# Kernel tuning notes

Hardware: AMD Instinct MI355X
Metric: run time of the kernel (lower is better)

The kernel has to match this reference:

```python
import jax, jax.numpy as jnp
import numpy as np
from jax import lax

CAP_N = 3
ROUTE_NUM = 3


def squash(s, axis=-1):
    # v = (|s|^2 / (1+|s|^2)) * s / |s|
    n2 = jnp.sum(s * s, axis=axis, keepdims=True)
    return (n2 / (1.0 + n2)) * s * lax.rsqrt(n2 + 1e-8)


def cap_layer2(x, W, bias, b0, num_out_caps, out_dim, as_final):
    # x: [bs, in_dim, H, W]; W: [out_dim*num_out_caps, in_dim] (1x1 conv)
    bs = x.shape[0]
    pred = jnp.einsum('oc,bchw->bohw', W, x) + bias[None, :, None, None]
    pred = pred.reshape(bs, num_out_caps, out_dim, -1)      # [bs, out_caps, d, in_caps]
    pred = jnp.transpose(pred, (0, 3, 1, 2))                # [bs, in_caps, out_caps, d]
    b = b0                                                   # [bs, out_caps, in_caps]
    v = None
    for _ in range(ROUTE_NUM):
        c = jax.nn.softmax(b, axis=1)                        # softmax over out_caps
        s = jnp.einsum('boi,biod->bod', c, pred)             # [bs, out_caps, d]
        v = squash(s)
        db = lax.stop_gradient(jnp.einsum('bod,biod->boi', v, pred))
        b = b + db
    if not as_final:
        side = int(np.sqrt(num_out_caps))
        v = jnp.transpose(v, (0, 2, 1)).reshape(bs, out_dim, side, side)
    return v


def setup_inputs() -> dict:
    key = jax.random.key(0)
    ks = jax.random.split(key, 8)
    bs = 128
    x = jax.random.normal(ks[0], (bs, 64, 8, 8), dtype=jnp.float32)
    Wb = jax.random.normal(ks[1], (64, 64, 3, 3), dtype=jnp.float32) * 0.05
    bb = jnp.zeros((64,), dtype=jnp.float32)
    W1 = jax.random.normal(ks[2], (4096, 64), dtype=jnp.float32) * 0.05
    b1 = jnp.zeros((4096,), dtype=jnp.float32)
    W2 = jax.random.normal(ks[3], (640, 64), dtype=jnp.float32) * 0.05
    b2 = jnp.zeros((640,), dtype=jnp.float32)
    b_basic = jax.random.uniform(ks[4], (CAP_N, bs, 64, 64), dtype=jnp.float32)
    b_cls = jax.random.uniform(ks[5], (bs, 10, 64), dtype=jnp.float32)
    return {'x': x, 'Wb': Wb, 'bb': bb, 'W1': W1, 'b1': b1, 'W2': W2, 'b2': b2,
            'b_basic': b_basic, 'b_cls': b_cls}


def reference(x, Wb, bb, W1, b1, W2, b2, b_basic, b_cls):
    # buffer: 3x3 conv + ReLU
    h = lax.conv_general_dilated(x, Wb, (1, 1), 'SAME',
                                 dimension_numbers=('NCHW', 'OIHW', 'NCHW'))
    h = jax.nn.relu(h + bb[None, :, None, None])
    # _do_squash over channel dim per spatial location
    h = squash(h, axis=1)
    for i in range(CAP_N):
        h = cap_layer2(h, W1, b1, b_basic[i], 64, 64, False)
    v = cap_layer2(h, W2, b2, b_cls, 10, 64, True)   # [bs, 10, 64]
    return v
```

## Files before the change

### kernel.cpp

```cpp
#include <hip/hip_runtime.h>
#include <math.h>
#include <type_traits>


#define SYS_ST(p, v) __hip_atomic_store((p), (v), __ATOMIC_RELAXED, __HIP_MEMORY_SCOPE_SYSTEM)
#define SYS_LD(p)    __hip_atomic_load((p), __ATOMIC_RELAXED, __HIP_MEMORY_SCOPE_SYSTEM)

typedef float v4f __attribute__((ext_vector_type(4)));

__device__ __forceinline__ void sys_st4(float* p, float4 q) {
    v4f v; v[0] = q.x; v[1] = q.y; v[2] = q.z; v[3] = q.w;
    asm volatile("global_store_dwordx4 %0, %1, off sc0 sc1" :: "v"(p), "v"(v) : "memory");
}

__global__ __launch_bounds__(512) void prep_kernel(
    const float* __restrict__ x, const float* __restrict__ Wb,
    const float* __restrict__ bb,
    const float* __restrict__ W1, const float* __restrict__ b1,
    const float* __restrict__ W2, const float* __restrict__ b2,
    const float* __restrict__ b_basic,
    float* __restrict__ h,
    float* __restrict__ WT1, float* __restrict__ G1,
    float* __restrict__ gb1, float* __restrict__ bb21,
    float* __restrict__ WT2, float* __restrict__ G2,
    float* __restrict__ gb2, float* __restrict__ bb22,
    float* __restrict__ den0, int* __restrict__ flags)
{
    __shared__ float smem[10560];
    const int blk = blockIdx.x;
    const int t = threadIdx.x;

    if (blk < 128) {
        float* xs  = smem;
        float* hs  = smem + 6400;
        float* scl = smem + 10496;
        const int b = blk;
        for (int idx = t; idx < 6400; idx += 512) xs[idx] = 0.f;
        __syncthreads();
        #pragma unroll
        for (int k = 0; k < 2; ++k) {
            int idx4 = t + k * 512;
            float4 v = *(const float4*)&x[(size_t)b * 4096 + idx4 * 4];
            int e0 = idx4 * 4;
            int c  = e0 >> 6;
            int hw = e0 & 63;
            int r = hw >> 3, cc = hw & 7;
            float* xp = &xs[c * 100 + (r + 1) * 10 + (cc + 1)];
            xp[0] = v.x; xp[1] = v.y; xp[2] = v.z; xp[3] = v.w;
        }
        __syncthreads();
        const int oc = t >> 3;
        const int hg = t & 7;
        float acc[8];
        #pragma unroll
        for (int k = 0; k < 8; ++k) acc[k] = 0.f;
        const float* wp = Wb + (size_t)oc * 576;
        for (int ic = 0; ic < 64; ++ic) {
            float w[9];
            #pragma unroll
            for (int j = 0; j < 9; ++j) w[j] = wp[ic * 9 + j];
            const float* xr = &xs[ic * 100];
            #pragma unroll
            for (int k = 0; k < 8; ++k) {
                int hw = hg * 8 + k;
                int r = hw >> 3, cc = hw & 7;
                int p0 = r * 10 + cc;
                float a = acc[k];
                a = fmaf(w[0], xr[p0],      a);
                a = fmaf(w[1], xr[p0 + 1],  a);
                a = fmaf(w[2], xr[p0 + 2],  a);
                a = fmaf(w[3], xr[p0 + 10], a);
                a = fmaf(w[4], xr[p0 + 11], a);
                a = fmaf(w[5], xr[p0 + 12], a);
                a = fmaf(w[6], xr[p0 + 20], a);
                a = fmaf(w[7], xr[p0 + 21], a);
                a = fmaf(w[8], xr[p0 + 22], a);
                acc[k] = a;
            }
        }
        float bias = bb[oc];
        #pragma unroll
        for (int k = 0; k < 8; ++k) {
            float v = acc[k] + bias;
            hs[oc * 64 + hg * 8 + k] = v > 0.f ? v : 0.f;
        }
        __syncthreads();
        if (t < 64) {
            float n2 = 0.f;
            for (int c = 0; c < 64; ++c) { float v = hs[c * 64 + t]; n2 = fmaf(v, v, n2); }
            scl[t] = (n2 / (1.f + n2)) * rsqrtf(n2 + 1e-8f);
        }
        __syncthreads();
        #pragma unroll
        for (int k = 0; k < 2; ++k) {
            int idx4 = t + k * 512;
            int e0 = idx4 * 4;
            int hw0 = e0 & 63;
            float4 o;
            o.x = hs[e0 + 0] * scl[hw0 + 0];
            o.y = hs[e0 + 1] * scl[hw0 + 1];
            o.z = hs[e0 + 2] * scl[hw0 + 2];
            o.w = hs[e0 + 3] * scl[hw0 + 3];
            *(float4*)&h[(size_t)b * 4096 + e0] = o;
        }
    } else if (blk < 202) {
        const bool w1 = blk < 192;
        const int o = w1 ? (blk - 128) : (blk - 192);
        const float* W    = w1 ? W1 : W2;
        const float* bias = w1 ? b1 : b2;
        float* WT  = w1 ? WT1  : WT2;
        float* G   = w1 ? G1   : G2;
        float* gb  = w1 ? gb1  : gb2;
        float* bb2 = w1 ? bb21 : bb22;
        float* WS = smem;
        if (t < 256) {
            #pragma unroll
            for (int p = 0; p < 4; ++p) {
                int idx = t + p * 256;
                int d = idx >> 4, c0 = (idx & 15) * 4;
                *(float4*)&WS[d * 68 + c0] =
                    *(const float4*)&W[((size_t)o * 64 + d) * 64 + c0];
            }
        }
        __syncthreads();
        if (t < 256) {
            {
                const int Q = t & 15, R = t >> 4;
                #pragma unroll
                for (int p = 0; p < 4; ++p) {
                    int c = R + 16 * p;
                    float4 v;
                    v.x = WS[(4 * Q + 0) * 68 + c];
                    v.y = WS[(4 * Q + 1) * 68 + c];
                    v.z = WS[(4 * Q + 2) * 68 + c];
                    v.w = WS[(4 * Q + 3) * 68 + c];
                    *(float4*)&WT[((size_t)o * 64 + c) * 64 + 4 * Q] = v;
                }
            }
            {
                const int c1 = t >> 2, j = t & 3;
                float acc[16];
                #pragma unroll
                for (int g = 0; g < 16; ++g) acc[g] = 0.f;
                for (int d = 0; d < 64; ++d) {
                    float a = WS[d * 68 + c1];
                    #pragma unroll
                    for (int g = 0; g < 16; ++g)
                        acc[g] = fmaf(a, WS[d * 68 + j * 16 + g], acc[g]);
                }
                #pragma unroll
                for (int g = 0; g < 16; ++g)
                    G[(size_t)o * 4096 + c1 * 64 + j * 16 + g] = acc[g];
            }
            if (t < 64) {
                float s = 0.f;
                for (int d = 0; d < 64; ++d) s = fmaf(bias[o * 64 + d], WS[d * 68 + t], s);
                gb[o * 64 + t] = s;
            }
            if (t == 0) {
                float s = 0.f;
                for (int d = 0; d < 64; ++d) { float bv = bias[o * 64 + d]; s = fmaf(bv, bv, s); }
                bb2[o] = s;
            }
        }
    } else if (blk < 250) {
        const int g = (blk - 202) * 512 + t;
        const int L = g >> 13, b = (g >> 6) & 127, i = g & 63;
        const float* bp = b_basic + (((size_t)L * 128 + b) << 12) + i;
        float s = 0.f;
        for (int o = 0; o < 64; ++o) s += expf(bp[o * 64]);
        den0[((size_t)L * 128 + b) * 64 + i] = s;
    } else {
        for (int i = t; i < 4096; i += 512) flags[i] = 0;
    }
}

__global__ __launch_bounds__(1024, 4) void caps_fused(
    const float* __restrict__ h0,
    const float* __restrict__ WT1, const float* __restrict__ G1,
    const float* __restrict__ gb1, const float* __restrict__ bb21,
    const float* __restrict__ b1,
    const float* __restrict__ WT2, const float* __restrict__ G2,
    const float* __restrict__ gb2, const float* __restrict__ bb22,
    const float* __restrict__ b2,
    const float* __restrict__ b_basic, const float* __restrict__ b_cls,
    const float* __restrict__ den0,
    float* __restrict__ xbuf,
    float* __restrict__ vbuf,
    int*   __restrict__ flags,
    float* __restrict__ out)
{
    __shared__ float HC[8704];
    __shared__ float CC[2048];
    __shared__ float PP[10240];

    const int B    = blockIdx.x;
    const int q    = B >> 6;
    const int p    = B & 63;
    const int t    = threadIdx.x;
    const int wv   = t >> 6;
    const int lane = t & 63;
    const int Q    = lane & 15;
    const int GG   = lane >> 4;
    int step = 1, dcnt = 0;

    #pragma unroll
    for (int s = 0; s < 2; ++s) {
        float4 v = *(const float4*)&h0[(size_t)(2 * p + s) * 4096 + t * 4];
        int c = t >> 4, i0 = (t & 15) * 4;
        *(float4*)&HC[s * 4352 + c * 68 + i0] = v;
    }

    auto layer = [&](auto finc, const float* __restrict__ WT,
                     const float* __restrict__ Gm,
                     const float* __restrict__ gbp,
                     const float* __restrict__ bb2p,
                     const float* __restrict__ biasp,
                     const float* __restrict__ bsrc,
                     const float* __restrict__ den0p, bool entry) {
        constexpr bool FIN = decltype(finc)::value;
        const int o   = FIN ? wv : q * 16 + wv;
        const bool act = !FIN || wv < 10;
        const int row0 = (wv * 2) * 64, row1 = (wv * 2 + 1) * 64;

        float bl0 = 0.f, bl1 = 0.f, bb2o = 0.f;
        float4 gbv4 = make_float4(0.f, 0.f, 0.f, 0.f);
        float4 bias4 = gbv4;
        const float* pG  = Gm;
        const float* pWT = WT;
        if (act) {
            pG  = Gm + o * 4096 + GG * 64 + 4 * Q;
            pWT = WT + o * 4096 + GG * 64 + 4 * Q;
            gbv4 = *(const float4*)&gbp[o * 64 + 4 * Q];
            bb2o = bb2p[o];
            bias4 = *(const float4*)&biasp[o * 64 + 4 * Q];
            if (FIN) {
                bl0 = b_cls[(size_t)(2 * p) * 640 + o * 64 + lane];
                bl1 = b_cls[(size_t)(2 * p + 1) * 640 + o * 64 + lane];
            } else {
                bl0 = bsrc[o * 64 + lane];
                bl1 = bsrc[4096 + o * 64 + lane];
            }
        }

        if (entry) {
            if (t < 3) {
                int qq = t + (t >= q);
                while (SYS_LD(&flags[(qq * 64 + p) * 16]) < step) {}
            }
            __syncthreads();
            #pragma unroll
            for (int j = 0; j < 3; ++j) {
                int qq = j + (j >= q);
                const float* vp = vbuf + (size_t)(qq * 64 + p) * 2048;
                #pragma unroll
                for (int rep = 0; rep < 2; ++rep) {
                    int idx = rep * 1024 + t;
                    int d = idx & 63, s = (idx >> 6) & 1, ol = idx >> 7;
                    HC[s * 4352 + d * 68 + qq * 16 + ol] = SYS_LD(&vp[idx]);
                }
            }
            ++step;
            __syncthreads();
        } else {
            __syncthreads();
        }

        for (int it = 0; it < 3; ++it) {
            float cc0 = 0.f, cc1 = 0.f, bp0 = 1.f, bp1 = 1.f;
            if (act) { cc0 = expf(bl0); cc1 = expf(bl1); }
            if (it == 0 && !FIN) {
                if (act) { bp0 = den0p[lane]; bp1 = den0p[64 + lane]; }
            } else {
                PP[wv * 64 + lane] = cc0;
                PP[1024 + wv * 64 + lane] = cc1;
                __syncthreads();
                bp0 = 0.f; bp1 = 0.f;
                #pragma unroll
                for (int w = 0; w < 16; ++w) {
                    bp0 += PP[w * 64 + lane];
                    bp1 += PP[1024 + w * 64 + lane];
                }
                if (!FIN) {
                    float* xb = xbuf + ((size_t)(dcnt & 1) * 256 + B) * 128;
                    if (wv == 0) {
                        SYS_ST(&xb[lane], bp0);
                        SYS_ST(&xb[64 + lane], bp1);
                        asm volatile("s_waitcnt vmcnt(0)" ::: "memory");
                        if (lane == 0) SYS_ST(&flags[B * 16], step);
                        if (lane < 3) {
                            int qq = lane + (lane >= q);
                            while (SYS_LD(&flags[(qq * 64 + p) * 16]) < step) {}
                        }
                    }
                    __syncthreads();
                    #pragma unroll
                    for (int j = 0; j < 3; ++j) {
                        int qq = j + (j >= q);
                        const float* xp = xbuf + ((size_t)(dcnt & 1) * 256 + qq * 64 + p) * 128;
                        bp0 += SYS_LD(&xp[lane]);
                        bp1 += SYS_LD(&xp[64 + lane]);
                    }
                    ++step; ++dcnt;
                }
            }
            float sc0 = 0.f, sc1 = 0.f;
            if (act) {
                float cv0 = cc0 / bp0, cv1 = cc1 / bp1;
                CC[row0 + lane] = cv0;
                CC[row1 + lane] = cv1;
                float a0 = cv0, a1 = cv1;
                #pragma unroll
                for (int m = 1; m < 64; m <<= 1) {
                    a0 += __shfl_xor(a0, m, 64);
                    a1 += __shfl_xor(a1, m, 64);
                }
                sc0 = a0; sc1 = a1;
            }
            __builtin_amdgcn_wave_barrier();

            float y0 = 0.f, y1 = 0.f;
            if (act) {
                #pragma unroll 8
                for (int k = 0; k < 16; ++k) {
                    float4 h40 = *(const float4*)&HC[lane * 68 + 4 * k];
                    float4 c40 = *(const float4*)&CC[row0 + 4 * k];
                    y0 = fmaf(h40.x, c40.x, y0); y0 = fmaf(h40.y, c40.y, y0);
                    y0 = fmaf(h40.z, c40.z, y0); y0 = fmaf(h40.w, c40.w, y0);
                    float4 h41 = *(const float4*)&HC[4352 + lane * 68 + 4 * k];
                    float4 c41 = *(const float4*)&CC[row1 + 4 * k];
                    y1 = fmaf(h41.x, c41.x, y1); y1 = fmaf(h41.y, c41.y, y1);
                    y1 = fmaf(h41.z, c41.z, y1); y1 = fmaf(h41.w, c41.w, y1);
                }
            }
            __builtin_amdgcn_wave_barrier();
            if (act) { CC[row0 + lane] = y0; CC[row1 + lane] = y1; }
            __builtin_amdgcn_wave_barrier();

            if (it < 2) {
                float4 a0 = make_float4(0.f, 0.f, 0.f, 0.f), a1 = a0;
                if (act) {
                    #pragma unroll 8
                    for (int k = 0; k < 16; ++k) {
                        float4 w4 = *(const float4*)&pG[k << 8];
                        float yb0 = CC[row0 + 4 * k + GG];
                        float yb1 = CC[row1 + 4 * k + GG];
                        a0.x = fmaf(w4.x, yb0, a0.x); a0.y = fmaf(w4.y, yb0, a0.y);
                        a0.z = fmaf(w4.z, yb0, a0.z); a0.w = fmaf(w4.w, yb0, a0.w);
                        a1.x = fmaf(w4.x, yb1, a1.x); a1.y = fmaf(w4.y, yb1, a1.y);
                        a1.z = fmaf(w4.z, yb1, a1.z); a1.w = fmaf(w4.w, yb1, a1.w);
                    }
                    #pragma unroll
                    for (int m = 16; m <= 32; m <<= 1) {
                        a0.x += __shfl_xor(a0.x, m, 64); a0.y += __shfl_xor(a0.y, m, 64);
                        a0.z += __shfl_xor(a0.z, m, 64); a0.w += __shfl_xor(a0.w, m, 64);
                        a1.x += __shfl_xor(a1.x, m, 64); a1.y += __shfl_xor(a1.y, m, 64);
                        a1.z += __shfl_xor(a1.z, m, 64); a1.w += __shfl_xor(a1.w, m, 64);
                    }
                }
                float vd0 = 0.f, vd1 = 0.f;
                if (act) {
                    float4 y40 = *(const float4*)&CC[row0 + 4 * Q];
                    float4 y41 = *(const float4*)&CC[row1 + 4 * Q];
                    float n20 = y40.x * a0.x + y40.y * a0.y + y40.z * a0.z + y40.w * a0.w;
                    float n21 = y41.x * a1.x + y41.y * a1.y + y41.z * a1.z + y41.w * a1.w;
                    float yg0 = y40.x * gbv4.x + y40.y * gbv4.y + y40.z * gbv4.z + y40.w * gbv4.w;
                    float yg1 = y41.x * gbv4.x + y41.y * gbv4.y + y41.z * gbv4.z + y41.w * gbv4.w;
                    #pragma unroll
                    for (int m = 1; m <= 8; m <<= 1) {
                        n20 += __shfl_xor(n20, m, 64);
                        n21 += __shfl_xor(n21, m, 64);
                        yg0 += __shfl_xor(yg0, m, 64);
                        yg1 += __shfl_xor(yg1, m, 64);
                    }
                    n20 = n20 + 2.f * sc0 * yg0 + sc0 * sc0 * bb2o;
                    n21 = n21 + 2.f * sc1 * yg1 + sc1 * sc1 * bb2o;
                    float s0 = (n20 / (1.f + n20)) * rsqrtf(n20 + 1e-8f);
                    float s1 = (n21 / (1.f + n21)) * rsqrtf(n21 + 1e-8f);
                    vd0 = s0 * (yg0 + sc0 * bb2o);
                    vd1 = s1 * (yg1 + sc1 * bb2o);
                    if (GG == 0) {
                        float4 u0, u1;
                        u0.x = s0 * (a0.x + sc0 * gbv4.x); u0.y = s0 * (a0.y + sc0 * gbv4.y);
                        u0.z = s0 * (a0.z + sc0 * gbv4.z); u0.w = s0 * (a0.w + sc0 * gbv4.w);
                        u1.x = s1 * (a1.x + sc1 * gbv4.x); u1.y = s1 * (a1.y + sc1 * gbv4.y);
                        u1.z = s1 * (a1.z + sc1 * gbv4.z); u1.w = s1 * (a1.w + sc1 * gbv4.w);
                        *(float4*)&CC[row0 + 4 * Q] = u0;
                        *(float4*)&CC[row1 + 4 * Q] = u1;
                    }
                }
                __builtin_amdgcn_wave_barrier();

                if (act) {
                    float4 d0 = make_float4(0.f, 0.f, 0.f, 0.f), d1 = d0;
                    #pragma unroll 8
                    for (int k = 0; k < 16; ++k) {
                        int c = 4 * k + GG;
                        float4 hc0 = *(const float4*)&HC[c * 68 + 4 * Q];
                        float ub0 = CC[row0 + c];
                        d0.x = fmaf(ub0, hc0.x, d0.x); d0.y = fmaf(ub0, hc0.y, d0.y);
                        d0.z = fmaf(ub0, hc0.z, d0.z); d0.w = fmaf(ub0, hc0.w, d0.w);
                        float4 hc1 = *(const float4*)&HC[4352 + c * 68 + 4 * Q];
                        float ub1 = CC[row1 + c];
                        d1.x = fmaf(ub1, hc1.x, d1.x); d1.y = fmaf(ub1, hc1.y, d1.y);
                        d1.z = fmaf(ub1, hc1.z, d1.z); d1.w = fmaf(ub1, hc1.w, d1.w);
                    }
                    #pragma unroll
                    for (int m = 16; m <= 32; m <<= 1) {
                        d0.x += __shfl_xor(d0.x, m, 64); d0.y += __shfl_xor(d0.y, m, 64);
                        d0.z += __shfl_xor(d0.z, m, 64); d0.w += __shfl_xor(d0.w, m, 64);
                        d1.x += __shfl_xor(d1.x, m, 64); d1.y += __shfl_xor(d1.y, m, 64);
                        d1.z += __shfl_xor(d1.z, m, 64); d1.w += __shfl_xor(d1.w, m, 64);
                    }
                    if (GG == 0) {
                        *(float4*)&CC[row0 + 4 * Q] = d0;
                        *(float4*)&CC[row1 + 4 * Q] = d1;
                    }
                }
                __builtin_amdgcn_wave_barrier();
                if (act) {
                    bl0 += CC[row0 + lane] + vd0;
                    bl1 += CC[row1 + lane] + vd1;
                }
            } else {
                if (act) {
                    float4 s40 = make_float4(0.f, 0.f, 0.f, 0.f), s41 = s40;
                    #pragma unroll 8
                    for (int k = 0; k < 16; ++k) {
                        float4 w4 = *(const float4*)&pWT[k << 8];
                        float yb0 = CC[row0 + 4 * k + GG];
                        float yb1 = CC[row1 + 4 * k + GG];
                        s40.x = fmaf(w4.x, yb0, s40.x); s40.y = fmaf(w4.y, yb0, s40.y);
                        s40.z = fmaf(w4.z, yb0, s40.z); s40.w = fmaf(w4.w, yb0, s40.w);
                        s41.x = fmaf(w4.x, yb1, s41.x); s41.y = fmaf(w4.y, yb1, s41.y);
                        s41.z = fmaf(w4.z, yb1, s41.z); s41.w = fmaf(w4.w, yb1, s41.w);
                    }
                    #pragma unroll
                    for (int m = 16; m <= 32; m <<= 1) {
                        s40.x += __shfl_xor(s40.x, m, 64); s40.y += __shfl_xor(s40.y, m, 64);
                        s40.z += __shfl_xor(s40.z, m, 64); s40.w += __shfl_xor(s40.w, m, 64);
                        s41.x += __shfl_xor(s41.x, m, 64); s41.y += __shfl_xor(s41.y, m, 64);
                        s41.z += __shfl_xor(s41.z, m, 64); s41.w += __shfl_xor(s41.w, m, 64);
                    }
                    s40.x = fmaf(bias4.x, sc0, s40.x); s40.y = fmaf(bias4.y, sc0, s40.y);
                    s40.z = fmaf(bias4.z, sc0, s40.z); s40.w = fmaf(bias4.w, sc0, s40.w);
                    s41.x = fmaf(bias4.x, sc1, s41.x); s41.y = fmaf(bias4.y, sc1, s41.y);
                    s41.z = fmaf(bias4.z, sc1, s41.z); s41.w = fmaf(bias4.w, sc1, s41.w);
                    float n20 = s40.x * s40.x + s40.y * s40.y + s40.z * s40.z + s40.w * s40.w;
                    float n21 = s41.x * s41.x + s41.y * s41.y + s41.z * s41.z + s41.w * s41.w;
                    #pragma unroll
                    for (int m = 1; m <= 8; m <<= 1) {
                        n20 += __shfl_xor(n20, m, 64);
                        n21 += __shfl_xor(n21, m, 64);
                    }
                    float sl0 = (n20 / (1.f + n20)) * rsqrtf(n20 + 1e-8f);
                    float sl1 = (n21 / (1.f + n21)) * rsqrtf(n21 + 1e-8f);
                    float4 v0, v1;
                    v0.x = s40.x * sl0; v0.y = s40.y * sl0; v0.z = s40.z * sl0; v0.w = s40.w * sl0;
                    v1.x = s41.x * sl1; v1.y = s41.y * sl1; v1.z = s41.z * sl1; v1.w = s41.w * sl1;
                    if (FIN) {
                        if (q == 0 && GG == 0) {
                            *(float4*)&out[(size_t)(2 * p) * 640 + o * 64 + 4 * Q] = v0;
                            *(float4*)&out[(size_t)(2 * p + 1) * 640 + o * 64 + 4 * Q] = v1;
                        }
                    } else if (GG == 0) {
                        *(float4*)&CC[row0 + 4 * Q] = v0;
                        *(float4*)&CC[row1 + 4 * Q] = v1;
                    }
                }
            }
        }

        if (!FIN) {
            __syncthreads();
            float* vb = vbuf + (size_t)B * 2048;
            if (t < 512)
                sys_st4(&vb[t * 4], *(const float4*)&CC[t * 4]);
            asm volatile("s_waitcnt vmcnt(0)" ::: "memory");
            __syncthreads();
            if (t == 0) SYS_ST(&flags[B * 16], step);
            #pragma unroll
            for (int rep = 0; rep < 2; ++rep) {
                int idx = rep * 1024 + t;
                int d = idx & 63, s = (idx >> 6) & 1, ol = idx >> 7;
                HC[s * 4352 + d * 68 + q * 16 + ol] = CC[idx];
            }
            __syncthreads();
        }
    };

    layer(std::integral_constant<bool, false>{}, WT1, G1, gb1, bb21, b1,
          b_basic + (((size_t)0 * 128 + 2 * p) << 12),
          den0 + ((size_t)0 * 128 + 2 * p) * 64, false);
    layer(std::integral_constant<bool, false>{}, WT1, G1, gb1, bb21, b1,
          b_basic + (((size_t)1 * 128 + 2 * p) << 12),
          den0 + ((size_t)1 * 128 + 2 * p) * 64, true);
    layer(std::integral_constant<bool, false>{}, WT1, G1, gb1, bb21, b1,
          b_basic + (((size_t)2 * 128 + 2 * p) << 12),
          den0 + ((size_t)2 * 128 + 2 * p) * 64, true);
    layer(std::integral_constant<bool, true>{}, WT2, G2, gb2, bb22, b2,
          nullptr, nullptr, true);
}

extern "C" void kernel_launch(void* const* d_in, const int* in_sizes, int n_in,
                              void* d_out, int out_size, void* d_ws, size_t ws_size,
                              hipStream_t stream) {
    const float* x       = (const float*)d_in[0];
    const float* Wb      = (const float*)d_in[1];
    const float* bb      = (const float*)d_in[2];
    const float* W1      = (const float*)d_in[3];
    const float* b1      = (const float*)d_in[4];
    const float* W2      = (const float*)d_in[5];
    const float* b2      = (const float*)d_in[6];
    const float* b_basic = (const float*)d_in[7];
    const float* b_cls   = (const float*)d_in[8];
    float* out = (float*)d_out;

    float* h0    = (float*)d_ws;
    float* WT1   = h0   + 524288;
    float* WT2   = WT1  + 262144;
    float* G1    = WT2  + 40960;
    float* G2    = G1   + 262144;
    float* gb1   = G2   + 40960;
    float* gb2   = gb1  + 4096;
    float* bb21  = gb2  + 640;
    float* bb22  = bb21 + 64;
    float* den0  = bb22 + 16;
    float* xbuf  = den0 + 24576;
    float* vbuf  = xbuf + 65536;
    int*   flags = (int*)(vbuf + 524288);

    prep_kernel<<<251, 512, 0, stream>>>(x, Wb, bb, W1, b1, W2, b2, b_basic,
                                         h0, WT1, G1, gb1, bb21,
                                         WT2, G2, gb2, bb22, den0, flags);
    caps_fused<<<256, 1024, 0, stream>>>(h0, WT1, G1, gb1, bb21, b1,
                                         WT2, G2, gb2, bb22, b2,
                                         b_basic, b_cls, den0,
                                         xbuf, vbuf, flags, out);
}
```

Baseline: 140.3 us.

## Split prep conv across half-blocks and keep transposed H copy in LDS

```diff
diff --git a/kernel.cpp b/kernel.cpp
--- a/kernel.cpp
+++ b/kernel.cpp
@@ -26,86 +26,13 @@
     float* __restrict__ gb2, float* __restrict__ bb22,
     float* __restrict__ den0, int* __restrict__ flags)
 {
-    __shared__ float smem[10560];
+    __shared__ float smem[8480];
     const int blk = blockIdx.x;
     const int t = threadIdx.x;
 
-    if (blk < 128) {
-        float* xs  = smem;
-        float* hs  = smem + 6400;
-        float* scl = smem + 10496;
-        const int b = blk;
-        for (int idx = t; idx < 6400; idx += 512) xs[idx] = 0.f;
-        __syncthreads();
-        #pragma unroll
-        for (int k = 0; k < 2; ++k) {
-            int idx4 = t + k * 512;
-            float4 v = *(const float4*)&x[(size_t)b * 4096 + idx4 * 4];
-            int e0 = idx4 * 4;
-            int c  = e0 >> 6;
-            int hw = e0 & 63;
-            int r = hw >> 3, cc = hw & 7;
-            float* xp = &xs[c * 100 + (r + 1) * 10 + (cc + 1)];
-            xp[0] = v.x; xp[1] = v.y; xp[2] = v.z; xp[3] = v.w;
-        }
-        __syncthreads();
-        const int oc = t >> 3;
-        const int hg = t & 7;
-        float acc[8];
-        #pragma unroll
-        for (int k = 0; k < 8; ++k) acc[k] = 0.f;
-        const float* wp = Wb + (size_t)oc * 576;
-        for (int ic = 0; ic < 64; ++ic) {
-            float w[9];
-            #pragma unroll
-            for (int j = 0; j < 9; ++j) w[j] = wp[ic * 9 + j];
-            const float* xr = &xs[ic * 100];
-            #pragma unroll
-            for (int k = 0; k < 8; ++k) {
-                int hw = hg * 8 + k;
-                int r = hw >> 3, cc = hw & 7;
-                int p0 = r * 10 + cc;
-                float a = acc[k];
-                a = fmaf(w[0], xr[p0],      a);
-                a = fmaf(w[1], xr[p0 + 1],  a);
-                a = fmaf(w[2], xr[p0 + 2],  a);
-                a = fmaf(w[3], xr[p0 + 10], a);
-                a = fmaf(w[4], xr[p0 + 11], a);
-                a = fmaf(w[5], xr[p0 + 12], a);
-                a = fmaf(w[6], xr[p0 + 20], a);
-                a = fmaf(w[7], xr[p0 + 21], a);
-                a = fmaf(w[8], xr[p0 + 22], a);
-                acc[k] = a;
-            }
-        }
-        float bias = bb[oc];
-        #pragma unroll
-        for (int k = 0; k < 8; ++k) {
-            float v = acc[k] + bias;
-            hs[oc * 64 + hg * 8 + k] = v > 0.f ? v : 0.f;
-        }
-        __syncthreads();
-        if (t < 64) {
-            float n2 = 0.f;
-            for (int c = 0; c < 64; ++c) { float v = hs[c * 64 + t]; n2 = fmaf(v, v, n2); }
-            scl[t] = (n2 / (1.f + n2)) * rsqrtf(n2 + 1e-8f);
-        }
-        __syncthreads();
-        #pragma unroll
-        for (int k = 0; k < 2; ++k) {
-            int idx4 = t + k * 512;
-            int e0 = idx4 * 4;
-            int hw0 = e0 & 63;
-            float4 o;
-            o.x = hs[e0 + 0] * scl[hw0 + 0];
-            o.y = hs[e0 + 1] * scl[hw0 + 1];
-            o.z = hs[e0 + 2] * scl[hw0 + 2];
-            o.w = hs[e0 + 3] * scl[hw0 + 3];
-            *(float4*)&h[(size_t)b * 4096 + e0] = o;
-        }
-    } else if (blk < 202) {
-        const bool w1 = blk < 192;
-        const int o = w1 ? (blk - 128) : (blk - 192);
+    if (blk < 74) {
+        const bool w1 = blk < 64;
+        const int o = w1 ? blk : (blk - 64);
         const float* W    = w1 ? W1 : W2;
         const float* bias = w1 ? b1 : b2;
         float* WT  = w1 ? WT1  : WT2;
@@ -163,15 +90,83 @@
                 bb2[o] = s;
             }
         }
-    } else if (blk < 250) {
-        const int g = (blk - 202) * 512 + t;
+    } else if (blk < 122) {
+        const int g = (blk - 74) * 512 + t;
         const int L = g >> 13, b = (g >> 6) & 127, i = g & 63;
         const float* bp = b_basic + (((size_t)L * 128 + b) << 12) + i;
         float s = 0.f;
         for (int o = 0; o < 64; ++o) s += expf(bp[o * 64]);
         den0[((size_t)L * 128 + b) * 64 + i] = s;
+    } else if (blk == 122) {
+        for (int i = t; i < 4096; i += 512) flags[i] = 0;
     } else {
-        for (int i = t; i < 4096; i += 512) flags[i] = 0;
+        float* xs  = smem;
+        float* hs  = smem + 6400;
+        float* scl = smem + 8448;
+        const int id = blk - 123;
+        const int b = id >> 1, hh = id & 1;
+        for (int idx = t; idx < 6400; idx += 512) xs[idx] = 0.f;
+        __syncthreads();
+        #pragma unroll
+        for (int k2 = 0; k2 < 2; ++k2) {
+            int idx4 = t + k2 * 512;
+            float4 v = *(const float4*)&x[(size_t)b * 4096 + idx4 * 4];
+            int e0 = idx4 * 4;
+            int c  = e0 >> 6;
+            int hw = e0 & 63;
+            int r = hw >> 3, cc = hw & 7;
+            float* xp = &xs[c * 100 + (r + 1) * 10 + (cc + 1)];
+            xp[0] = v.x; xp[1] = v.y; xp[2] = v.z; xp[3] = v.w;
+        }
+        __syncthreads();
+        const int oc = t >> 3;
+        const int hg = t & 7;
+        float acc[4] = {0.f, 0.f, 0.f, 0.f};
+        const float* wp = Wb + (size_t)oc * 576;
+        for (int ic = 0; ic < 64; ++ic) {
+            float w[9];
+            #pragma unroll
+            for (int j = 0; j < 9; ++j) w[j] = wp[ic * 9 + j];
+            const float* xr = &xs[ic * 100];
+            #pragma unroll
+            for (int k = 0; k < 4; ++k) {
+                int hw = hh * 32 + hg * 4 + k;
+                int r = hw >> 3, cc = hw & 7;
+                int p0 = r * 10 + cc;
+                float a = acc[k];
+                a = fmaf(w[0], xr[p0],      a);
+                a = fmaf(w[1], xr[p0 + 1],  a);
+                a = fmaf(w[2], xr[p0 + 2],  a);
+                a = fmaf(w[3], xr[p0 + 10], a);
+                a = fmaf(w[4], xr[p0 + 11], a);
+                a = fmaf(w[5], xr[p0 + 12], a);
+                a = fmaf(w[6], xr[p0 + 20], a);
+                a = fmaf(w[7], xr[p0 + 21], a);
+                a = fmaf(w[8], xr[p0 + 22], a);
+                acc[k] = a;
+            }
+        }
+        float bias = bb[oc];
+        #pragma unroll
+        for (int k = 0; k < 4; ++k) {
+            float v = acc[k] + bias;
+            hs[oc * 32 + hg * 4 + k] = v > 0.f ? v : 0.f;
+        }
+        __syncthreads();
+        if (t < 32) {
+            float n2 = 0.f;
+            for (int c = 0; c < 64; ++c) { float v = hs[c * 32 + t]; n2 = fmaf(v, v, n2); }
+            scl[t] = (n2 / (1.f + n2)) * rsqrtf(n2 + 1e-8f);
+        }
+        __syncthreads();
+        {
+            float4 o;
+            o.x = hs[oc * 32 + hg * 4 + 0] * scl[hg * 4 + 0];
+            o.y = hs[oc * 32 + hg * 4 + 1] * scl[hg * 4 + 1];
+            o.z = hs[oc * 32 + hg * 4 + 2] * scl[hg * 4 + 2];
+            o.w = hs[oc * 32 + hg * 4 + 3] * scl[hg * 4 + 3];
+            *(float4*)&h[(size_t)b * 4096 + oc * 64 + hh * 32 + hg * 4] = o;
+        }
     }
 }
 
@@ -191,8 +186,9 @@
     float* __restrict__ out)
 {
     __shared__ float HC[8704];
+    __shared__ float HT[8192];
     __shared__ float CC[2048];
-    __shared__ float PP[10240];
+    __shared__ float PP[2048];
 
     const int B    = blockIdx.x;
     const int q    = B >> 6;
@@ -209,6 +205,10 @@
         float4 v = *(const float4*)&h0[(size_t)(2 * p + s) * 4096 + t * 4];
         int c = t >> 4, i0 = (t & 15) * 4;
         *(float4*)&HC[s * 4352 + c * 68 + i0] = v;
+        HT[s * 4096 + (i0 + 0) * 64 + c] = v.x;
+        HT[s * 4096 + (i0 + 1) * 64 + c] = v.y;
+        HT[s * 4096 + (i0 + 2) * 64 + c] = v.z;
+        HT[s * 4096 + (i0 + 3) * 64 + c] = v.w;
     }
 
     auto layer = [&](auto finc, const float* __restrict__ WT,
@@ -257,7 +257,9 @@
                 for (int rep = 0; rep < 2; ++rep) {
                     int idx = rep * 1024 + t;
                     int d = idx & 63, s = (idx >> 6) & 1, ol = idx >> 7;
-                    HC[s * 4352 + d * 68 + qq * 16 + ol] = SYS_LD(&vp[idx]);
+                    float v = SYS_LD(&vp[idx]);
+                    HC[s * 4352 + d * 68 + qq * 16 + ol] = v;
+                    HT[s * 4096 + (qq * 16 + ol) * 64 + d] = v;
                 }
             }
             ++step;
@@ -323,14 +325,18 @@
             if (act) {
                 #pragma unroll 8
                 for (int k = 0; k < 16; ++k) {
-                    float4 h40 = *(const float4*)&HC[lane * 68 + 4 * k];
                     float4 c40 = *(const float4*)&CC[row0 + 4 * k];
-                    y0 = fmaf(h40.x, c40.x, y0); y0 = fmaf(h40.y, c40.y, y0);
-                    y0 = fmaf(h40.z, c40.z, y0); y0 = fmaf(h40.w, c40.w, y0);
-                    float4 h41 = *(const float4*)&HC[4352 + lane * 68 + 4 * k];
                     float4 c41 = *(const float4*)&CC[row1 + 4 * k];
-                    y1 = fmaf(h41.x, c41.x, y1); y1 = fmaf(h41.y, c41.y, y1);
-                    y1 = fmaf(h41.z, c41.z, y1); y1 = fmaf(h41.w, c41.w, y1);
+                    const float* hp0 = &HT[(4 * k) * 64 + lane];
+                    const float* hp1 = &HT[4096 + (4 * k) * 64 + lane];
+                    y0 = fmaf(c40.x, hp0[0],   y0);
+                    y0 = fmaf(c40.y, hp0[64],  y0);
+                    y0 = fmaf(c40.z, hp0[128], y0);
+                    y0 = fmaf(c40.w, hp0[192], y0);
+                    y1 = fmaf(c41.x, hp1[0],   y1);
+                    y1 = fmaf(c41.y, hp1[64],  y1);
+                    y1 = fmaf(c41.z, hp1[128], y1);
+                    y1 = fmaf(c41.w, hp1[192], y1);
                 }
             }
             __builtin_amdgcn_wave_barrier();
@@ -483,7 +489,9 @@
             for (int rep = 0; rep < 2; ++rep) {
                 int idx = rep * 1024 + t;
                 int d = idx & 63, s = (idx >> 6) & 1, ol = idx >> 7;
-                HC[s * 4352 + d * 68 + q * 16 + ol] = CC[idx];
+                float v = CC[idx];
+                HC[s * 4352 + d * 68 + q * 16 + ol] = v;
+                HT[s * 4096 + (q * 16 + ol) * 64 + d] = v;
             }
             __syncthreads();
         }
@@ -530,7 +538,7 @@
     float* vbuf  = xbuf + 65536;
     int*   flags = (int*)(vbuf + 524288);
 
-    prep_kernel<<<251, 512, 0, stream>>>(x, Wb, bb, W1, b1, W2, b2, b_basic,
+    prep_kernel<<<379, 512, 0, stream>>>(x, Wb, bb, W1, b1, W2, b2, b_basic,
                                          h0, WT1, G1, gb1, bb21,
                                          WT2, G2, gb2, bb22, den0, flags);
     caps_fused<<<256, 1024, 0, stream>>>(h0, WT1, G1, gb1, bb21, b1,
```

Result: no change. 141.8 us (+1.0%).
